# Optimization experiments

Hardware: AMD Instinct MI355X
Metric: run time of the kernel (lower is better)

Reference implementation:

```python
import jax, jax.numpy as jnp
import numpy as np

B, H, W, E = 8, 64, 64, 256  # channels == embedding (required by final Multiply)


def setup_inputs() -> dict:
    key = jax.random.key(0)
    k1, k2, k3 = jax.random.split(key, 3)
    inputs = jax.random.normal(k1, (B, H, W, E), dtype=jnp.float32)
    # Conv2D(embedding, 3, padding='same') params, HWIO layout
    conv_w = jax.random.normal(k2, (3, 3, E, E), dtype=jnp.float32) * (1.0 / np.sqrt(9 * E))
    conv_b = jnp.zeros((E,), dtype=jnp.float32)
    return {"inputs": inputs, "conv_w": conv_w, "conv_b": conv_b}


def reference(inputs, conv_w, conv_b):
    emb = conv_w.shape[-1]
    # conv1: 3x3 same-padded conv, NHWC
    x = jax.lax.conv_general_dilated(
        inputs, conv_w, window_strides=(1, 1), padding="SAME",
        dimension_numbers=("NHWC", "HWIO", "NHWC")) + conv_b
    b, h, w, e = x.shape
    x1 = x.reshape(b, h * w, e)                       # [B, N, E]
    scores = jnp.einsum("bne,bme->bnm", x1, x1)       # [B, N, N]
    attn = jax.nn.softmax(scores, axis=-1) / jnp.sqrt(jnp.asarray(emb, x.dtype))
    out = jnp.einsum("bnm,bme->bne", attn, x1)        # [B, N, E]
    # Original keras uses Reshape((inputs.shape[-2], inputs.shape[-3], -1)): (W, H, E)
    out = out.reshape(b, w, h, e)
    return out * inputs
```

## Files before the change

### kernel.cpp

```cpp
#include <hip/hip_runtime.h>
#include <hip/hip_bf16.h>

typedef __attribute__((ext_vector_type(4))) float f32x4;
typedef __attribute__((ext_vector_type(8))) _Float16 f16x8;
typedef __attribute__((ext_vector_type(16))) float f32x16;
typedef unsigned short u16;

#define NB 8
#define NE 256
#define NN 4096
#define SD 64

__device__ __forceinline__ f32x16 z16() {
  f32x16 v;
#pragma unroll
  for (int i = 0; i < 16; ++i) v[i] = 0.f;
  return v;
}
__device__ __forceinline__ void gload_lds16(const void* g, void* l) {
  __builtin_amdgcn_global_load_lds((const __attribute__((address_space(1))) void*)g,
                                   (__attribute__((address_space(3))) void*)l, 16, 0, 0);
}
__device__ __forceinline__ float fexp2(float x) {
#if __has_builtin(__builtin_amdgcn_exp2f)
  return __builtin_amdgcn_exp2f(x);
#else
  return exp2f(x);
#endif
}

#if __has_builtin(__builtin_amdgcn_permlane32_swap)
typedef int i32x2 __attribute__((ext_vector_type(2)));
__device__ __forceinline__ void plswap(int& a, int& b) {
  i32x2 r = __builtin_amdgcn_permlane32_swap(a, b, false, false);
  a = r[0]; b = r[1];
}
#else
__device__ __forceinline__ void plswap(int& a, int& b) {
  int xa = __shfl_xor(a, 32), xb = __shfl_xor(b, 32);
  int hi = (int)((threadIdx.x & 63) >> 5);
  int na = hi ? xb : a;
  int nb = hi ? b : xa;
  a = na; b = nb;
}
#endif

__global__ __launch_bounds__(256) void k_prep(const float* __restrict__ x, u16* __restrict__ outF,
                                              const float* __restrict__ w, u16* __restrict__ wT) {
  int bid = blockIdx.x;
  int tid = threadIdx.x;
  if (bid < 8192) {
    int i = bid * 256 + tid;
    float4 v = reinterpret_cast<const float4*>(x)[i];
    ushort4 o;
    o.x = __builtin_bit_cast(u16, (_Float16)v.x);
    o.y = __builtin_bit_cast(u16, (_Float16)v.y);
    o.z = __builtin_bit_cast(u16, (_Float16)v.z);
    o.w = __builtin_bit_cast(u16, (_Float16)v.w);
    reinterpret_cast<ushort4*>(outF)[i] = o;
  } else {
    int i = (bid - 8192) * 256 + tid;
    int t = i >> 16;
    int r = i & 65535;
    int ei = r >> 8, eo = r & 255;
    int o = (t << 16) + (eo << 8) + ei;
    wT[o] = __builtin_bit_cast(u16, (_Float16)w[i]);
  }
}

__global__ __launch_bounds__(256, 2) void k_conv(const u16* __restrict__ inF,
                                                 const u16* __restrict__ wT,
                                                 const float* __restrict__ bias,
                                                 u16* __restrict__ x1h) {
  __shared__ u16 Ahalo[264 * 64];
  __shared__ u16 BhL[2][128 * 64];
  int b = blockIdx.x >> 6;
  int rem = blockIdx.x & 63;
  int mt = rem >> 1, et = rem & 1;
  int h0 = mt << 1;
  int tid = threadIdx.x;
  int wid = tid >> 6, lane = tid & 63;
  int wr = wid >> 1, wc = wid & 1;
  int r = lane & 15, g = lane >> 4;
  f32x4 acc[4][4];
#pragma unroll
  for (int i = 0; i < 4; ++i)
#pragma unroll
    for (int j = 0; j < 4; ++j) acc[i][j] = (f32x4){0.f, 0.f, 0.f, 0.f};
  const long ibase = (long)b * NN * NE;

  const int bsw = ((((lane & 7) << 4) ^ (((lane >> 3) & 7) << 4)) >> 1);
  long bSrc[4];
#pragma unroll
  for (int i = 0; i < 4; ++i) {
    int c = wid * 4 + i;
    int eo = c * 8 + (lane >> 3);
    bSrc[i] = (long)(et * 128 + eo) * 256 + bsw;
  }
  int aSlot[9], aHalo[9];
  const u16* aSrc[9];
#pragma unroll
  for (int j = 0; j < 9; ++j) {
    int c = wid + 4 * j;
    int slot = c * 8 + (lane >> 3);
    int hr = slot >= 198 ? 3 : (slot >= 132 ? 2 : (slot >= 66 ? 1 : 0));
    int hc = slot - hr * 66;
    int ir = h0 - 1 + hr, ic = hc - 1;
    aHalo[j] = ((unsigned)ir >= 64u) | ((unsigned)ic >= 64u);
    int irc = min(max(ir, 0), 63), icc = min(max(ic, 0), 63);
    int c8s = (lane & 7) ^ (slot & 7);
    aSlot[j] = slot;
    aSrc[j] = inF + ibase + ((long)(irc * 64 + icc) << 8) + c8s * 8;
  }

#pragma unroll
  for (int i = 0; i < 4; ++i)
    gload_lds16(wT + bSrc[i], (char*)BhL[0] + (wid * 4 + i) * 1024);

#pragma unroll 1
  for (int kc = 0; kc < 4; ++kc) {
    __builtin_amdgcn_s_barrier();
#pragma unroll
    for (int j = 0; j < 9; ++j) {
      int c = wid + 4 * j;
      if (c < 33)
        gload_lds16(aSrc[j] + kc * 64, (char*)Ahalo + c * 1024);
    }
    asm volatile("s_waitcnt vmcnt(0)" ::: "memory");
#pragma unroll
    for (int j = 0; j < 9; ++j) {
      int c = wid + 4 * j;
      if (c < 33 && aHalo[j])
        *reinterpret_cast<float4*>((char*)Ahalo + c * 1024 + (lane << 4)) =
            make_float4(0.f, 0.f, 0.f, 0.f);
    }
    asm volatile("s_waitcnt lgkmcnt(0)" ::: "memory");
    __builtin_amdgcn_s_barrier();

#pragma unroll 1
    for (int t = 0; t < 9; ++t) {
      int gidx = kc * 9 + t;
      if (t > 0) {
        asm volatile("s_waitcnt vmcnt(0)" ::: "memory");
        __builtin_amdgcn_s_barrier();
      }
      if (gidx < 35) {
        int nt = t + 1 == 9 ? 0 : t + 1;
        int nkc = t + 1 == 9 ? kc + 1 : kc;
        long tkoff = ((long)nt << 16) + nkc * 64;
        char* dstB = (char*)BhL[(gidx + 1) & 1];
#pragma unroll
        for (int i = 0; i < 4; ++i)
          gload_lds16(wT + tkoff + bSrc[i], dstB + (wid * 4 + i) * 1024);
      }
      const u16* BB = BhL[gidx & 1];
      int dy = t / 3 - 1, dx = t % 3 - 1;
      int abase = (wr + 1 + dy) * 66 + 1 + dx;
#pragma unroll
      for (int ks = 0; ks < 2; ++ks) {
        int c8 = ks * 4 + g;
        f16x8 ah[4], bh[4];
#pragma unroll
        for (int mi = 0; mi < 4; ++mi) {
          int slot = abase + mi * 16 + r;
          int abyte = (slot << 7) + ((c8 << 4) ^ ((slot & 7) << 4));
          ah[mi] = *reinterpret_cast<const f16x8*>(reinterpret_cast<const char*>(Ahalo) + abyte);
        }
#pragma unroll
        for (int ni = 0; ni < 4; ++ni) {
          int col = wc * 64 + ni * 16 + r;
          int bbyte = (col << 7) + ((c8 << 4) ^ ((r & 7) << 4));
          bh[ni] = *reinterpret_cast<const f16x8*>(reinterpret_cast<const char*>(BB) + bbyte);
        }
#pragma unroll
        for (int mi = 0; mi < 4; ++mi)
#pragma unroll
          for (int ni = 0; ni < 4; ++ni)
            acc[mi][ni] = __builtin_amdgcn_mfma_f32_16x16x32_f16(ah[mi], bh[ni], acc[mi][ni], 0, 0, 0);
      }
    }
  }
#pragma unroll
  for (int mi = 0; mi < 4; ++mi)
#pragma unroll
    for (int ni = 0; ni < 4; ++ni) {
      int eo = et * 128 + wc * 64 + ni * 16 + r;
      float bz = bias[eo];
#pragma unroll
      for (int i = 0; i < 4; ++i) {
        int pix = mt * 128 + wr * 64 + mi * 16 + g * 4 + i;
        float v = acc[mi][ni][i] + bz;
        long o = ibase + (long)pix * NE + eo;
        x1h[o] = __builtin_bit_cast(u16, (_Float16)v);
      }
    }
}

__global__ __launch_bounds__(256) void k_trans(const u16* __restrict__ x1h, u16* __restrict__ x1T) {
  __shared__ u16 T[64][72];
  int bid = blockIdx.x;
  int b = bid >> 8, rem = bid & 255;
  int mt = rem >> 2, et = rem & 3;
  int tid = threadIdx.x;
  for (int c = tid; c < 512; c += 256) {
    int rr = c >> 3, c8 = c & 7;
    *reinterpret_cast<float4*>(&T[rr][c8 * 8]) =
        *reinterpret_cast<const float4*>(x1h + ((long)b * NN + mt * 64 + rr) * NE + et * 64 + c8 * 8);
  }
  __syncthreads();
  for (int c = tid; c < 512; c += 256) {
    int er = c >> 3, m8 = c & 7;
    union { u16 u[8]; float4 v; } p;
#pragma unroll
    for (int j = 0; j < 8; ++j) p.u[j] = T[m8 * 8 + j][er];
    *reinterpret_cast<float4*>(x1T + ((long)b * NE + et * 64 + er) * NN + mt * 64 + m8 * 8) = p.v;
  }
}

__global__ __launch_bounds__(256, 2) void k_flash3(const u16* __restrict__ x1h16,
                                                   const u16* __restrict__ x1T,
                                                   const float* __restrict__ inp,
                                                   float* __restrict__ out) {
  __shared__ char LDS[65536];
  int phys = blockIdx.x;
  int b = phys & 7;
  int qt = phys >> 3;
  int tid = threadIdx.x, wid = tid >> 6, lane = tid & 63;
  int r31 = lane & 31, hi = lane >> 5;
  int eh = wid & 1, qg = wid >> 1;
  const long bN = (long)b << 12;
  const long vtb = (long)b << 20;

  const long qrow = bN + qt * 64 + qg * 32 + r31;
  f16x8 qh[16];
#pragma unroll
  for (int ks = 0; ks < 16; ++ks) {
    qh[ks] = *reinterpret_cast<const f16x8*>(x1h16 + (qrow << 8) + ks * 16 + hi * 8);
#pragma unroll
    for (int j = 0; j < 8; ++j)
      qh[ks][j] = (_Float16)((float)qh[ks][j] * 1.44269504f);
  }

  f32x16 o4[4];
#pragma unroll
  for (int nf = 0; nf < 4; ++nf) o4[nf] = z16();
  float mrow = -1.0e30f, lrow = 0.f;

  const u16* kS[4];
  const u16* vS[4];
  int off[4];
#pragma unroll
  for (int i = 0; i < 4; ++i) {
    int c = wid * 4 + i;
    off[i] = c << 10;
    int kr = c * 2 + (lane >> 5);
    int kcolb = ((lane & 31) << 4) ^ ((kr & 15) << 4);
    kS[i] = x1h16 + ((bN + kr) << 8) + (kcolb >> 1);
    int rp = c * 16 + (lane >> 2);
    int e = rp ^ ((rp >> 2) & 1);
    int vcolb = ((lane & 3) << 4) ^ ((e & 3) << 4);
    vS[i] = x1T + vtb + ((long)e << 12) + (vcolb >> 1);
  }

#pragma unroll
  for (int i = 0; i < 4; ++i) { gload_lds16(kS[i], LDS + off[i]); kS[i] += 8192; }
#pragma unroll
  for (int i = 0; i < 4; ++i) { gload_lds16(vS[i], LDS + 32768 + off[i]); vS[i] += 32; }

#pragma unroll 1
  for (int it = 0; it < 128; ++it) {
    const char* KB = LDS + (it & 1) * 16384;
    const char* VB = LDS + 32768 + (it & 1) * 16384;

    asm volatile("s_waitcnt vmcnt(0)" ::: "memory");
    __builtin_amdgcn_s_barrier();
    __builtin_amdgcn_sched_barrier(0);

    if (it < 127) {
      char* KD = LDS + ((it + 1) & 1) * 16384;
      char* VD = LDS + 32768 + ((it + 1) & 1) * 16384;
#pragma unroll
      for (int i = 0; i < 4; ++i) { gload_lds16(kS[i], KD + off[i]); kS[i] += 8192; }
#pragma unroll
      for (int i = 0; i < 4; ++i) { gload_lds16(vS[i], VD + off[i]); vS[i] += 32; }
    }

    f32x16 stA = z16(), stB = z16();
    int swzk = (r31 & 15) << 4;
    int krow = r31 << 9;
    __builtin_amdgcn_s_setprio(1);
#pragma unroll
    for (int ks = 0; ks < 8; ++ks) {
      int cbyA = ((2 * ks) * 32 + hi * 16) ^ swzk;
      int cbyB = ((2 * ks + 1) * 32 + hi * 16) ^ swzk;
      f16x8 kA = *reinterpret_cast<const f16x8*>(KB + krow + cbyA);
      f16x8 kB = *reinterpret_cast<const f16x8*>(KB + krow + cbyB);
      stA = __builtin_amdgcn_mfma_f32_32x32x16_f16(kA, qh[2 * ks], stA, 0, 0, 0);
      stB = __builtin_amdgcn_mfma_f32_32x32x16_f16(kB, qh[2 * ks + 1], stB, 0, 0, 0);
    }
    __builtin_amdgcn_s_setprio(0);
    f32x16 st;
#pragma unroll
    for (int m = 0; m < 16; ++m) st[m] = stA[m] + stB[m];

    float t8[8];
#pragma unroll
    for (int m = 0; m < 8; ++m) t8[m] = fmaxf(st[m], st[m + 8]);
    float t4a = fmaxf(t8[0], t8[4]), t4b = fmaxf(t8[1], t8[5]);
    float t4c = fmaxf(t8[2], t8[6]), t4d = fmaxf(t8[3], t8[7]);
    float tmax = fmaxf(fmaxf(t4a, t4b), fmaxf(t4c, t4d));
    tmax = fmaxf(tmax, __shfl_xor(tmax, 32));
    if (!__all(tmax <= mrow + 11.54f)) {
      float mnew = fmaxf(mrow, tmax);
      float alpha = fexp2(mrow - mnew);
      lrow *= alpha;
      float ar[16];
#pragma unroll
      for (int m = 0; m < 16; ++m) ar[m] = __shfl(alpha, (m & 3) + 8 * (m >> 2) + 4 * hi);
#pragma unroll
      for (int nf = 0; nf < 4; ++nf)
#pragma unroll
        for (int m = 0; m < 16; ++m) o4[nf][m] *= ar[m];
      mrow = mnew;
    }
#pragma unroll
    for (int m = 0; m < 16; ++m) st[m] = fexp2(st[m] - mrow);
    float s8[8];
#pragma unroll
    for (int m = 0; m < 8; ++m) s8[m] = st[m] + st[m + 8];
    float s4a = s8[0] + s8[4], s4b = s8[1] + s8[5], s4c = s8[2] + s8[6], s4d = s8[3] + s8[7];
    float psum = (s4a + s4b) + (s4c + s4d);
    psum += __shfl_xor(psum, 32);
    lrow += psum;

    int Wd[8];
#pragma unroll
    for (int m = 0; m < 8; ++m) {
      unsigned l0 = __builtin_bit_cast(u16, (_Float16)st[2 * m]);
      unsigned h0 = __builtin_bit_cast(u16, (_Float16)st[2 * m + 1]);
      Wd[m] = (int)(l0 | (h0 << 16));
    }
    plswap(Wd[0], Wd[2]); plswap(Wd[1], Wd[3]);
    plswap(Wd[4], Wd[6]); plswap(Wd[5], Wd[7]);
    union PU { int w[4]; f16x8 v; };
    PU pa[2];
#pragma unroll
    for (int c = 0; c < 2; ++c) {
      pa[c].w[0] = Wd[c * 4 + 0]; pa[c].w[1] = Wd[c * 4 + 1];
      pa[c].w[2] = Wd[c * 4 + 2]; pa[c].w[3] = Wd[c * 4 + 3];
    }

    __builtin_amdgcn_s_setprio(1);
#pragma unroll
    for (int nf = 0; nf < 4; ++nf) {
      int e = eh * 128 + nf * 32 + r31;
      const char* vrow = VB + ((e << 6) ^ ((e & 4) << 4));
      int swzv = (e & 3) << 4;
#pragma unroll
      for (int c = 0; c < 2; ++c) {
        f16x8 v = *reinterpret_cast<const f16x8*>(vrow + ((c * 32 + hi * 16) ^ swzv));
        o4[nf] = __builtin_amdgcn_mfma_f32_32x32x16_f16(pa[c].v, v, o4[nf], 0, 0, 0);
      }
    }
    __builtin_amdgcn_s_setprio(0);
  }

  float linv = 1.0f / (16.0f * lrow);
  float lr[16];
#pragma unroll
  for (int m = 0; m < 16; ++m) lr[m] = __shfl(linv, (m & 3) + 8 * (m >> 2) + 4 * hi);
  const long ob = (bN + qt * 64 + qg * 32) << 8;
#pragma unroll
  for (int nf = 0; nf < 4; ++nf)
#pragma unroll
    for (int m = 0; m < 16; ++m) {
      int qr = (m & 3) + 8 * (m >> 2) + 4 * hi;
      long off2 = ob + ((long)qr << 8) + eh * 128 + nf * 32 + r31;
      out[off2] = o4[nf][m] * lr[m] * inp[off2];
    }
}

extern "C" void kernel_launch(void* const* d_in, const int* in_sizes, int n_in,
                              void* d_out, int out_size, void* d_ws, size_t ws_size,
                              hipStream_t stream) {
  const float* inp   = (const float*)d_in[0];
  const float* convw = (const float*)d_in[1];
  const float* convb = (const float*)d_in[2];
  float* out = (float*)d_out;
  char* ws = (char*)d_ws;

  u16* x1h = (u16*)(ws);
  u16* x1T = (u16*)(ws + 16777216L);
  u16* inF = (u16*)(ws + 33554432L);
  u16* wT  = (u16*)(ws + 50331648L);

  k_prep<<<10496, 256, 0, stream>>>(inp, inF, convw, wT);
  k_conv<<<512, 256, 0, stream>>>(inF, wT, convb, x1h);
  k_trans<<<2048, 256, 0, stream>>>(x1h, x1T);
  k_flash3<<<512, 256, 0, stream>>>(x1h, x1T, inp, out);
}
```

Before: 306.8 us.

## Software-pipeline attention: overlap previous PV MFMAs with current QK scores

Restructures the flash-attention loop so the P·V MFMAs of iteration it-1 run right after the Q·K MFMAs of iteration it, with a final PV step after the loop. The aim is to let matrix work cover the softmax (exp, max, sum) latency instead of leaving it serialized. K and V prefetches are now issued separately, and V only after an extra barrier that keeps the previous V buffer safe to read. The cost is one more barrier per iteration and the P fragments staying live in registers across iterations. It also drops an unused array in the conv kernel.

```diff
diff --git a/kernel.cpp b/kernel.cpp
--- a/kernel.cpp
+++ b/kernel.cpp
@@ -97,7 +97,7 @@
     int eo = c * 8 + (lane >> 3);
     bSrc[i] = (long)(et * 128 + eo) * 256 + bsw;
   }
-  int aSlot[9], aHalo[9];
+  int aHalo[9];
   const u16* aSrc[9];
 #pragma unroll
   for (int j = 0; j < 9; ++j) {
@@ -109,7 +109,6 @@
     aHalo[j] = ((unsigned)ir >= 64u) | ((unsigned)ic >= 64u);
     int irc = min(max(ir, 0), 63), icc = min(max(ic, 0), 63);
     int c8s = (lane & 7) ^ (slot & 7);
-    aSlot[j] = slot;
     aSrc[j] = inF + ibase + ((long)(irc * 64 + icc) << 8) + c8s * 8;
   }
 
@@ -217,7 +216,7 @@
   }
 }
 
-__global__ __launch_bounds__(256, 2) void k_flash3(const u16* __restrict__ x1h16,
+__global__ __launch_bounds__(256, 2) void k_flash6(const u16* __restrict__ x1h16,
                                                    const u16* __restrict__ x1T,
                                                    const float* __restrict__ inp,
                                                    float* __restrict__ out) {
@@ -267,23 +266,17 @@
 #pragma unroll
   for (int i = 0; i < 4; ++i) { gload_lds16(vS[i], LDS + 32768 + off[i]); vS[i] += 32; }
 
+  union PU { int w[4]; f16x8 v; };
+  PU paP[2];
+
 #pragma unroll 1
   for (int it = 0; it < 128; ++it) {
     const char* KB = LDS + (it & 1) * 16384;
-    const char* VB = LDS + 32768 + (it & 1) * 16384;
+    const char* VBp = LDS + 32768 + ((it - 1) & 1) * 16384;
 
     asm volatile("s_waitcnt vmcnt(0)" ::: "memory");
     __builtin_amdgcn_s_barrier();
     __builtin_amdgcn_sched_barrier(0);
-
-    if (it < 127) {
-      char* KD = LDS + ((it + 1) & 1) * 16384;
-      char* VD = LDS + 32768 + ((it + 1) & 1) * 16384;
-#pragma unroll
-      for (int i = 0; i < 4; ++i) { gload_lds16(kS[i], KD + off[i]); kS[i] += 8192; }
-#pragma unroll
-      for (int i = 0; i < 4; ++i) { gload_lds16(vS[i], VD + off[i]); vS[i] += 32; }
-    }
 
     f32x16 stA = z16(), stB = z16();
     int swzk = (r31 & 15) << 4;
@@ -298,7 +291,27 @@
       stA = __builtin_amdgcn_mfma_f32_32x32x16_f16(kA, qh[2 * ks], stA, 0, 0, 0);
       stB = __builtin_amdgcn_mfma_f32_32x32x16_f16(kB, qh[2 * ks + 1], stB, 0, 0, 0);
     }
+    if (it > 0) {
+#pragma unroll
+      for (int nf = 0; nf < 4; ++nf) {
+        int e = eh * 128 + nf * 32 + r31;
+        const char* vrow = VBp + ((e << 6) ^ ((e & 4) << 4));
+        int swzv = (e & 3) << 4;
+#pragma unroll
+        for (int c = 0; c < 2; ++c) {
+          f16x8 v = *reinterpret_cast<const f16x8*>(vrow + ((c * 32 + hi * 16) ^ swzv));
+          o4[nf] = __builtin_amdgcn_mfma_f32_32x32x16_f16(paP[c].v, v, o4[nf], 0, 0, 0);
+        }
+      }
+    }
     __builtin_amdgcn_s_setprio(0);
+
+    if (it < 127) {
+      char* KD = LDS + ((it + 1) & 1) * 16384;
+#pragma unroll
+      for (int i = 0; i < 4; ++i) { gload_lds16(kS[i], KD + off[i]); kS[i] += 8192; }
+    }
+
     f32x16 st;
 #pragma unroll
     for (int m = 0; m < 16; ++m) st[m] = stA[m] + stB[m];
@@ -342,27 +355,33 @@
     }
     plswap(Wd[0], Wd[2]); plswap(Wd[1], Wd[3]);
     plswap(Wd[4], Wd[6]); plswap(Wd[5], Wd[7]);
-    union PU { int w[4]; f16x8 v; };
-    PU pa[2];
 #pragma unroll
     for (int c = 0; c < 2; ++c) {
-      pa[c].w[0] = Wd[c * 4 + 0]; pa[c].w[1] = Wd[c * 4 + 1];
-      pa[c].w[2] = Wd[c * 4 + 2]; pa[c].w[3] = Wd[c * 4 + 3];
-    }
-
-    __builtin_amdgcn_s_setprio(1);
+      paP[c].w[0] = Wd[c * 4 + 0]; paP[c].w[1] = Wd[c * 4 + 1];
+      paP[c].w[2] = Wd[c * 4 + 2]; paP[c].w[3] = Wd[c * 4 + 3];
+    }
+
+    __builtin_amdgcn_s_barrier();
+    if (it < 127) {
+      char* VD = LDS + 32768 + ((it + 1) & 1) * 16384;
+#pragma unroll
+      for (int i = 0; i < 4; ++i) { gload_lds16(vS[i], VD + off[i]); vS[i] += 32; }
+    }
+  }
+
+  {
+    const char* VBp = LDS + 32768 + (127 & 1) * 16384;
 #pragma unroll
     for (int nf = 0; nf < 4; ++nf) {
       int e = eh * 128 + nf * 32 + r31;
-      const char* vrow = VB + ((e << 6) ^ ((e & 4) << 4));
+      const char* vrow = VBp + ((e << 6) ^ ((e & 4) << 4));
       int swzv = (e & 3) << 4;
 #pragma unroll
       for (int c = 0; c < 2; ++c) {
         f16x8 v = *reinterpret_cast<const f16x8*>(vrow + ((c * 32 + hi * 16) ^ swzv));
-        o4[nf] = __builtin_amdgcn_mfma_f32_32x32x16_f16(pa[c].v, v, o4[nf], 0, 0, 0);
-      }
-    }
-    __builtin_amdgcn_s_setprio(0);
+        o4[nf] = __builtin_amdgcn_mfma_f32_32x32x16_f16(paP[c].v, v, o4[nf], 0, 0, 0);
+      }
+    }
   }
 
   float linv = 1.0f / (16.0f * lrow);
@@ -397,5 +416,5 @@
   k_prep<<<10496, 256, 0, stream>>>(inp, inF, convw, wT);
   k_conv<<<512, 256, 0, stream>>>(inF, wT, convb, x1h);
   k_trans<<<2048, 256, 0, stream>>>(x1h, x1T);
-  k_flash3<<<512, 256, 0, stream>>>(x1h, x1T, inp, out);
-}
+  k_flash6<<<512, 256, 0, stream>>>(x1h, x1T, inp, out);
+}
```

Result: slower. 314.4 us (+2.5%).
